# Optimization experiments

Measured on AMD Instinct MI355X. Metric: run time of the kernel, lower is better.

## Reference

```python
import jax, jax.numpy as jnp
import numpy as np

N, T, D = 32768, 2048, 2
CLAMP_SIGMA2_MIN = 1e-12


def setup_inputs() -> dict:
    key = jax.random.key(0)
    z = jax.random.normal(key, (N, T, D), dtype=jnp.float32)
    # per-dimension GARCH(1,1) parameters (stationary: alpha + beta < 1)
    omega = 0.05 * jnp.ones((D,), jnp.float32)
    alpha = 0.08 * jnp.ones((D,), jnp.float32)
    beta = 0.90 * jnp.ones((D,), jnp.float32)
    mu = jnp.zeros((D,), jnp.float32)
    sigma2_0 = jnp.ones((D,), jnp.float32)
    return {"z": z, "omega": omega, "alpha": alpha, "beta": beta,
            "mu": mu, "sigma2_0": sigma2_0}


def reference(z, omega, alpha, beta, mu, sigma2_0):
    # z: (N, T, d) iid noise; params: (d,). GARCH(1,1) per dimension:
    #   sigma_t^2 = omega + alpha * eps_{t-1}^2 + beta * sigma_{t-1}^2
    #   eps_t = sigma_t * z_t ;  x_t = mu + eps_t
    n, t, d = z.shape

    def step(carry, z_t):
        eps2_prev, sig2_prev = carry            # each (N, d)
        sig2 = omega + alpha * eps2_prev + beta * sig2_prev
        sig2 = jnp.maximum(sig2, CLAMP_SIGMA2_MIN)
        eps = jnp.sqrt(sig2) * z_t
        return (eps * eps, sig2), mu + eps

    eps2_init = jnp.zeros((n, d), z.dtype)
    sig2_init = jnp.broadcast_to(sigma2_0.astype(z.dtype), (n, d))
    _, x_tnd = jax.lax.scan(step, (eps2_init, sig2_init), jnp.swapaxes(z, 0, 1))
    return jnp.swapaxes(x_tnd, 0, 1)            # (N, T, d)
```

## Files before the change

kernel.cpp:

```cpp
#include <hip/hip_runtime.h>
#include <hip/hip_bf16.h>


#define GARCH_N 32768
#define GARCH_T 2048
#define F4_PER_CHAIN (GARCH_T * 2 / 4)
#define CHUNK 16
#define NCHUNK (F4_PER_CHAIN / CHUNK)

struct GarchState {
    float s2a, s2b, e2a, e2b;
    float o0, o1, a0, a1, b0, b1, m0, m1;
};

__device__ __forceinline__ void garch_chunk(const float4 (&in)[CHUNK],
                                            float4* __restrict__ xp, int c,
                                            GarchState& st)
{
    #pragma unroll
    for (int j = 0; j < CHUNK; ++j) {
        const float4 v = in[j];

        st.s2a = fmaf(st.b0, st.s2a, fmaf(st.a0, st.e2a, st.o0));
        st.s2a = fmaxf(st.s2a, 1e-12f);
        float ea = sqrtf(st.s2a) * v.x;
        float xa = st.m0 + ea;
        st.e2a = ea * ea;

        st.s2b = fmaf(st.b1, st.s2b, fmaf(st.a1, st.e2b, st.o1));
        st.s2b = fmaxf(st.s2b, 1e-12f);
        float eb = sqrtf(st.s2b) * v.y;
        float xb = st.m1 + eb;
        st.e2b = eb * eb;

        st.s2a = fmaf(st.b0, st.s2a, fmaf(st.a0, st.e2a, st.o0));
        st.s2a = fmaxf(st.s2a, 1e-12f);
        float ec = sqrtf(st.s2a) * v.z;
        float xc = st.m0 + ec;
        st.e2a = ec * ec;

        st.s2b = fmaf(st.b1, st.s2b, fmaf(st.a1, st.e2b, st.o1));
        st.s2b = fmaxf(st.s2b, 1e-12f);
        float ed = sqrtf(st.s2b) * v.w;
        float xd = st.m1 + ed;
        st.e2b = ed * ed;

        xp[c + j] = make_float4(xa, xb, xc, xd);
    }
}

__global__ __launch_bounds__(128) void garch_kernel(
    const float4* __restrict__ z4,
    const float* __restrict__ omega,
    const float* __restrict__ alpha,
    const float* __restrict__ beta,
    const float* __restrict__ mu,
    const float* __restrict__ sigma2_0,
    float4* __restrict__ x4)
{
    const int n = blockIdx.x * blockDim.x + threadIdx.x;
    if (n >= GARCH_N) return;

    GarchState st;
    st.o0 = omega[0]; st.o1 = omega[1];
    st.a0 = alpha[0]; st.a1 = alpha[1];
    st.b0 = beta[0];  st.b1 = beta[1];
    st.m0 = mu[0];    st.m1 = mu[1];
    st.s2a = sigma2_0[0]; st.s2b = sigma2_0[1];
    st.e2a = 0.0f;        st.e2b = 0.0f;

    const float4* __restrict__ zp = z4 + (size_t)n * F4_PER_CHAIN;
    float4* __restrict__ xp       = x4 + (size_t)n * F4_PER_CHAIN;

    float4 bufA[CHUNK], bufB[CHUNK];

    #pragma unroll
    for (int j = 0; j < CHUNK; ++j) bufA[j] = zp[j];

    for (int c = 0; c < NCHUNK; c += 2) {
        #pragma unroll
        for (int j = 0; j < CHUNK; ++j) bufB[j] = zp[(c + 1) * CHUNK + j];

        garch_chunk(bufA, xp, c * CHUNK, st);

        if (c + 2 < NCHUNK) {
            #pragma unroll
            for (int j = 0; j < CHUNK; ++j) bufA[j] = zp[(c + 2) * CHUNK + j];
        }

        garch_chunk(bufB, xp, (c + 1) * CHUNK, st);
    }
}

extern "C" void kernel_launch(void* const* d_in, const int* in_sizes, int n_in,
                              void* d_out, int out_size, void* d_ws, size_t ws_size,
                              hipStream_t stream)
{
    const float4* z4      = (const float4*)d_in[0];
    const float* omega    = (const float*)d_in[1];
    const float* alpha    = (const float*)d_in[2];
    const float* beta     = (const float*)d_in[3];
    const float* mu       = (const float*)d_in[4];
    const float* sigma2_0 = (const float*)d_in[5];
    float4* x4            = (float4*)d_out;

    const int block = 128;
    const int grid  = (GARCH_N + block - 1) / block;
    garch_kernel<<<grid, block, 0, stream>>>(z4, omega, alpha, beta, mu, sigma2_0, x4);
}
```

Measured before the change: 992.7 us.

## Stage path tiles through LDS with async global_load_lds and coalesced stores

Replaces per-thread strided float4 loads and stores along each path with block-cooperative staging. Each 64-thread block async-copies 16-float4 tiles from 64 paths into a double-buffered LDS area using global_load_lds, with an XOR-swizzled column layout. Each thread then runs its recurrence on its row in LDS, writes results back in place, and the tile is stored to global memory cooperatively. The intent is to turn uncoalesced per-path access into coalesced accesses and to overlap loads with compute. The cost is added LDS traffic, manual vmcnt waits, and smaller blocks of 64 threads.

```diff
diff --git a/kernel.cpp b/kernel.cpp
--- a/kernel.cpp
+++ b/kernel.cpp
@@ -2,23 +2,53 @@
 #include <hip/hip_bf16.h>
 
 
-#define GARCH_N 32768
-#define GARCH_T 2048
-#define F4_PER_CHAIN (GARCH_T * 2 / 4)
-#define CHUNK 16
-#define NCHUNK (F4_PER_CHAIN / CHUNK)
+#define NPATH      32768
+#define PPB        64
+#define F4_PATH    1024
+#define CF4        16
+#define NTILE      (F4_PATH / CF4)
+#define LDSF4      (PPB * CF4)
 
-struct GarchState {
-    float s2a, s2b, e2a, e2b;
-    float o0, o1, a0, a1, b0, b1, m0, m1;
-};
+struct GS { float s2a, s2b, e2a, e2b, o0, o1, a0, a1, b0, b1, m0, m1; };
 
-__device__ __forceinline__ void garch_chunk(const float4 (&in)[CHUNK],
-                                            float4* __restrict__ xp, int c,
-                                            GarchState& st)
+__device__ __forceinline__ void issueA(const float4* __restrict__ zb, float4* Lb,
+                                       int c, int w4, int s)
 {
     #pragma unroll
-    for (int j = 0; j < CHUNK; ++j) {
+    for (int i = 0; i < 16; ++i) {
+        const int r   = i * 4 + w4;
+        const int col = s ^ (r & 15);
+        const float4* src = zb + (size_t)r * F4_PATH + (size_t)c * CF4 + col;
+        __builtin_amdgcn_global_load_lds(
+            (const __attribute__((address_space(1))) void*)src,
+            (__attribute__((address_space(3))) void*)(Lb + i * 64),
+            16, 0, 0);
+    }
+}
+
+__device__ __forceinline__ void doC(float4* __restrict__ xb, const float4* Lb,
+                                    int c, int w, int w4, int s)
+{
+    float4 v[16];
+    #pragma unroll
+    for (int i = 0; i < 16; ++i) v[i] = Lb[i * 64 + w];
+    #pragma unroll
+    for (int i = 0; i < 16; ++i) {
+        const int r   = i * 4 + w4;
+        const int col = s ^ (r & 15);
+        xb[(size_t)r * F4_PATH + (size_t)c * CF4 + col] = v[i];
+    }
+}
+
+__device__ __forceinline__ void doB(float4* Lb, int w, GS& st)
+{
+    const int m = w & 15;
+    float4 in[16];
+    #pragma unroll
+    for (int j = 0; j < 16; ++j) in[j] = Lb[w * CF4 + (j ^ m)];
+
+    #pragma unroll
+    for (int j = 0; j < 16; ++j) {
         const float4 v = in[j];
 
         st.s2a = fmaf(st.b0, st.s2a, fmaf(st.a0, st.e2a, st.o0));
@@ -45,11 +75,20 @@
         float xd = st.m1 + ed;
         st.e2b = ed * ed;
 
-        xp[c + j] = make_float4(xa, xb, xc, xd);
+        in[j] = make_float4(xa, xb, xc, xd);
     }
+
+    #pragma unroll
+    for (int j = 0; j < 16; ++j) Lb[w * CF4 + (j ^ m)] = in[j];
 }
 
-__global__ __launch_bounds__(128) void garch_kernel(
+#define VMWAIT16() do {                                   \
+    __builtin_amdgcn_sched_barrier(0);                    \
+    asm volatile("s_waitcnt vmcnt(16)" ::: "memory");     \
+    __builtin_amdgcn_sched_barrier(0);                    \
+} while (0)
+
+__global__ __launch_bounds__(PPB) void garch_kernel(
     const float4* __restrict__ z4,
     const float* __restrict__ omega,
     const float* __restrict__ alpha,
@@ -58,10 +97,17 @@
     const float* __restrict__ sigma2_0,
     float4* __restrict__ x4)
 {
-    const int n = blockIdx.x * blockDim.x + threadIdx.x;
-    if (n >= GARCH_N) return;
+    __shared__ float4 lds[2][LDSF4];
 
-    GarchState st;
+    const int w  = threadIdx.x;
+    const int w4 = w >> 4;
+    const int s  = w & 15;
+
+    const size_t pbase = (size_t)blockIdx.x * PPB;
+    const float4* __restrict__ zb = z4 + pbase * F4_PATH;
+    float4* __restrict__ xb       = x4 + pbase * F4_PATH;
+
+    GS st;
     st.o0 = omega[0]; st.o1 = omega[1];
     st.a0 = alpha[0]; st.a1 = alpha[1];
     st.b0 = beta[0];  st.b1 = beta[1];
@@ -69,27 +115,19 @@
     st.s2a = sigma2_0[0]; st.s2b = sigma2_0[1];
     st.e2a = 0.0f;        st.e2b = 0.0f;
 
-    const float4* __restrict__ zp = z4 + (size_t)n * F4_PER_CHAIN;
-    float4* __restrict__ xp       = x4 + (size_t)n * F4_PER_CHAIN;
+    issueA(zb, &lds[0][0], 0, w4, s);
+    issueA(zb, &lds[1][0], 1, w4, s);
+    VMWAIT16();
+    doB(&lds[0][0], w, st);
 
-    float4 bufA[CHUNK], bufB[CHUNK];
-
-    #pragma unroll
-    for (int j = 0; j < CHUNK; ++j) bufA[j] = zp[j];
-
-    for (int c = 0; c < NCHUNK; c += 2) {
-        #pragma unroll
-        for (int j = 0; j < CHUNK; ++j) bufB[j] = zp[(c + 1) * CHUNK + j];
-
-        garch_chunk(bufA, xp, c * CHUNK, st);
-
-        if (c + 2 < NCHUNK) {
-            #pragma unroll
-            for (int j = 0; j < CHUNK; ++j) bufA[j] = zp[(c + 2) * CHUNK + j];
-        }
-
-        garch_chunk(bufB, xp, (c + 1) * CHUNK, st);
+    for (int k = 1; k < NTILE; ++k) {
+        doC(xb, &lds[(k - 1) & 1][0], k - 1, w, w4, s);
+        __builtin_amdgcn_sched_barrier(0);
+        issueA(zb, &lds[(k + 1) & 1][0], (k + 1) & (NTILE - 1), w4, s);
+        VMWAIT16();
+        doB(&lds[k & 1][0], w, st);
     }
+    doC(xb, &lds[(NTILE - 1) & 1][0], NTILE - 1, w, w4, s);
 }
 
 extern "C" void kernel_launch(void* const* d_in, const int* in_sizes, int n_in,
@@ -104,7 +142,7 @@
     const float* sigma2_0 = (const float*)d_in[5];
     float4* x4            = (float4*)d_out;
 
-    const int block = 128;
-    const int grid  = (GARCH_N + block - 1) / block;
+    const int block = PPB;
+    const int grid  = NPATH / PPB;
     garch_kernel<<<grid, block, 0, stream>>>(z4, omega, alpha, beta, mu, sigma2_0, x4);
 }
```

Result: faster. 971.7 us (-2.1%).
